# Kernel optimization log

Hardware: AMD Instinct MI355X
Metric: run time of the kernel (lower is better)

Reference implementation:

```python
import jax, jax.numpy as jnp
import numpy as np

B, V, F, H = 2, 5023, 9976, 256
CHUNK = 128
EPS = 1e-5
LIGHT_LOC = jnp.array([0.0, 1.0, 3.0], dtype=jnp.float32)   # PointLights(location)
AMB, DIFF, SPEC = 0.5, 0.3, 0.2 * 0.6                        # light amb/diff * mat(1.0); spec light*mat
SHININESS = 10.0
TEXEL = jnp.array([142.0, 179.0, 247.0], dtype=jnp.float32) / 255.0
BG = jnp.array([1.0, 1.0, 1.0], dtype=jnp.float32)


def setup_inputs():
    key = jax.random.key(0)
    k1, k2 = jax.random.split(key)
    vertices = jax.random.normal(k1, (B, V, 3), dtype=jnp.float32) * 0.05
    faces = jax.random.randint(k2, (F, 3), 0, V)
    # default camera built inside forward: R = diag(-1,1,-1), T = (0,0,2*scale)
    tm = jnp.array([[-1.0, 0.0, 0.0, 0.0],
                    [0.0, 1.0, 0.0, 0.0],
                    [0.0, 0.0, -1.0, 2.0]], dtype=jnp.float32)
    transform_matrix = jnp.tile(tm[None], (B, 1, 1))
    focal_length = jnp.full((B, 1), 12.0, dtype=jnp.float32)
    return {"vertices": vertices, "transform_matrix": transform_matrix,
            "focal_length": focal_length, "faces": faces}


def _normalize(v):
    return v / jnp.maximum(jnp.linalg.norm(v, axis=-1, keepdims=True), 1e-6)


def _render(vertices, transform_matrix, focal_length, faces):
    R = transform_matrix[:, :3, :3]
    T = transform_matrix[:, :3, 3]
    # pytorch3d row-vector convention: x_cam = x_world @ R + T
    verts_cam = jnp.einsum('bvi,bij->bvj', vertices, R) + T[:, None, :]
    zc = verts_cam[..., 2]                                    # view depth
    x_ndc = focal_length * verts_cam[..., 0] / zc             # fx*x/z (+px=0)
    y_ndc = focal_length * verts_cam[..., 1] / zc
    vndc = jnp.stack([x_ndc, y_ndc, zc], axis=-1)             # [B,V,3]

    # pixel centers in pytorch3d NDC (+x left, +y up); top-left pixel -> (+1-1/H, +1-1/H)
    ax = 1.0 - (2.0 * jnp.arange(H, dtype=jnp.float32) + 1.0) / H
    px = jnp.tile(ax[None, :], (H, 1)).reshape(-1)            # [P] columns
    py = jnp.tile(ax[:, None], (1, H)).reshape(-1)            # [P] rows
    P = H * H

    npad = (-F) % CHUNK
    faces_p = jnp.concatenate([faces, jnp.zeros((npad, 3), faces.dtype)], 0)
    fvalid = jnp.concatenate([jnp.ones((F,), bool), jnp.zeros((npad,), bool)])
    n_chunks = faces_p.shape[0] // CHUNK
    chunk_ids = jnp.arange(n_chunks * CHUNK, dtype=jnp.int32).reshape(n_chunks, CHUNK)

    def step(carry, fidx):
        best_z, bw0, bw1, bw2, best_face = carry
        tri = faces_p[fidx]                                   # [C,3]
        fv = vndc[:, tri]                                     # [B,C,3,3]
        def corner(k):
            return (fv[:, :, k, 0][..., None], fv[:, :, k, 1][..., None],
                    fv[:, :, k, 2][..., None])
        x0, y0, z0 = corner(0); x1, y1, z1 = corner(1); x2, y2, z2 = corner(2)
        z0s = jnp.where(z0 > EPS, z0, 1.0)
        z1s = jnp.where(z1 > EPS, z1, 1.0)
        z2s = jnp.where(z2 > EPS, z2, 1.0)
        den = (y1 - y2) * (x0 - x2) + (x2 - x1) * (y0 - y2)   # [B,C,1]
        ok = jnp.abs(den) > 1e-8
        dens = jnp.where(ok, den, 1.0)
        w0 = ((y1 - y2) * (px - x2) + (x2 - x1) * (py - y2)) / dens   # [B,C,P]
        w1 = ((y2 - y0) * (px - x2) + (x0 - x2) * (py - y2)) / dens
        w2 = 1.0 - w0 - w1
        inside = (w0 >= 0) & (w1 >= 0) & (w2 >= 0) & ok
        inside &= (z0 > EPS) & (z1 > EPS) & (z2 > EPS)
        inside &= fvalid[fidx][None, :, None]
        iz = w0 / z0s + w1 / z1s + w2 / z2s                    # perspective-correct 1/z
        good = inside & (iz > 1e-8)
        izs = jnp.where(good, iz, 1.0)
        zsafe = 1.0 / izs
        zpix = jnp.where(good, zsafe, jnp.inf)
        w0c = jnp.where(good, (w0 / z0s) * zsafe, 0.0)
        w1c = jnp.where(good, (w1 / z1s) * zsafe, 0.0)
        w2c = jnp.where(good, (w2 / z2s) * zsafe, 0.0)
        idx = jnp.argmin(zpix, axis=1)                         # [B,P]
        g = lambda a: jnp.take_along_axis(a, idx[:, None, :], axis=1)[:, 0]
        zmin = g(zpix)
        upd = zmin < best_z
        best_z = jnp.where(upd, zmin, best_z)
        bw0 = jnp.where(upd, g(w0c), bw0)
        bw1 = jnp.where(upd, g(w1c), bw1)
        bw2 = jnp.where(upd, g(w2c), bw2)
        best_face = jnp.where(upd, fidx[idx], best_face)
        return (best_z, bw0, bw1, bw2, best_face), None

    init = (jnp.full((B, P), jnp.inf, jnp.float32),
            jnp.zeros((B, P), jnp.float32), jnp.zeros((B, P), jnp.float32),
            jnp.zeros((B, P), jnp.float32), jnp.full((B, P), -1, jnp.int32))
    (best_z, bw0, bw1, bw2, best_face), _ = jax.lax.scan(jax.checkpoint(step), init, chunk_ids)

    mask = best_face >= 0                                      # [B,P]
    bary = jnp.stack([bw0, bw1, bw2], axis=-1)                 # [B,P,3]
    tri_sel = faces_p[jnp.clip(best_face, 0)]                  # [B,P,3]

    # area-weighted vertex normals (pytorch3d _compute_vertex_normals)
    fw = vertices[:, faces]                                    # [B,F,3,3]
    fn = jnp.cross(fw[:, :, 1] - fw[:, :, 0], fw[:, :, 2] - fw[:, :, 0])  # [B,F,3]
    vn = jnp.zeros_like(vertices).at[:, faces.reshape(-1)].add(jnp.repeat(fn, 3, axis=1))
    vn = _normalize(vn)

    gv = jax.vmap(lambda t, i: t[i])(vertices, tri_sel)        # [B,P,3,3] world pos
    gn = jax.vmap(lambda t, i: t[i])(vn, tri_sel)              # [B,P,3,3] normals
    pos = jnp.einsum('bpk,bpkc->bpc', bary, gv)
    nrm = _normalize(jnp.einsum('bpk,bpkc->bpc', bary, gn))

    cam_pos = -jnp.einsum('bj,bkj->bk', T, R)                  # camera center in world
    Ldir = _normalize(LIGHT_LOC - pos)
    Vdir = _normalize(cam_pos[:, None, :] - pos)
    cosNL = jnp.sum(nrm * Ldir, axis=-1)
    diffuse = DIFF * jax.nn.relu(cosNL)
    refl = 2.0 * cosNL[..., None] * nrm - Ldir
    spec = SPEC * jax.nn.relu(jnp.sum(Vdir * refl, axis=-1)) ** SHININESS
    rgb = TEXEL * (AMB + diffuse)[..., None] + spec[..., None] # [B,P,3]
    rgb = jnp.where(mask[..., None], rgb, BG)                  # hard_rgb_blend, bg=(1,1,1)

    images = rgb.reshape(B, H, H, 3).transpose(0, 3, 1, 2) * 255.0  # area-interp to same size = identity
    alpha = mask.astype(jnp.float32).reshape(B, 1, H, H)
    return images, alpha


def reference(vertices, transform_matrix, focal_length, faces):
    return _render(vertices, transform_matrix, focal_length, faces)
```

## Files before the change

### kernel.cpp

```cpp
#include <hip/hip_runtime.h>
#include <stdint.h>

#define H 256
#define PIX (H*H)
#define BATCH 2
#define NV 5023
#define NF 9976
#define EPS 1e-5f
#define CH 128
#define NBUCK 4096

typedef unsigned long long ull;
#define INF_KEY 0x7F800000FFFFFFFFULL

__device__ __forceinline__ float axf(int i) {
    return 1.0f - (2.0f * (float)i + 1.0f) / (float)H;
}

__device__ __forceinline__ float bf16snap(float x) {
    unsigned u = __float_as_uint(x);
    unsigned r = (u + 0x7FFFu + ((u >> 16) & 1u)) & 0xFFFF0000u;
    return __uint_as_float(r);
}

__device__ __forceinline__ int zbucket(float z) {
    int q = (int)floorf((z - 0.5f) * (4096.0f / 3.0f));
    return q < 0 ? 0 : (q > 4095 ? 4095 : q);
}
__device__ __forceinline__ float zbucket_lower(int q) {
    return (q == 0) ? 0.0f : 0.5f + (float)q * (3.0f / 4096.0f);
}

__global__ void face_setup(const float* __restrict__ verts, const float* __restrict__ tm,
                           const float* __restrict__ focal, const int* __restrict__ faces,
                           float* __restrict__ fd, float* __restrict__ zminArr) {
#pragma clang fp contract(off)
    int t = blockIdx.x * blockDim.x + threadIdx.x;
    if (t >= BATCH * NF) return;
    int b = t / NF, f = t % NF;
    const float* M = tm + b * 12;
    float fl = focal[b];
    float X[3], Y[3], Z[3];
#pragma unroll
    for (int k = 0; k < 3; k++) {
        int vi = faces[f * 3 + k];
        const float* v = verts + (b * NV + vi) * 3;
        float v0 = v[0], v1 = v[1], v2 = v[2];
        float c0 = ((v0 * M[0] + v1 * M[4]) + v2 * M[8])  + M[3];
        float c1 = ((v0 * M[1] + v1 * M[5]) + v2 * M[9])  + M[7];
        float c2 = ((v0 * M[2] + v1 * M[6]) + v2 * M[10]) + M[11];
        X[k] = (fl * c0) / c2;
        Y[k] = (fl * c1) / c2;
        Z[k] = c2;
    }
    float x0 = X[0], x1 = X[1], x2 = X[2];
    float y0 = Y[0], y1 = Y[1], y2 = Y[2];
    float z0 = Z[0], z1 = Z[1], z2 = Z[2];
    float den = (y1 - y2) * (x0 - x2) + (x2 - x1) * (y0 - y2);
    bool zv = (z0 > EPS) && (z1 > EPS) && (z2 > EPS);
    bool okS = zv && (fabsf(den) > 1e-8f);
    bool okR = zv && (fabsf(den) > 5e-9f);
    float xmn, xmx, ymn, ymx;
    if (okR) {
        float e01 = (x1 - x0) * (x1 - x0) + (y1 - y0) * (y1 - y0);
        float e12 = (x2 - x1) * (x2 - x1) + (y2 - y1) * (y2 - y1);
        float e20 = (x0 - x2) * (x0 - x2) + (y0 - y2) * (y0 - y2);
        float E2 = fmaxf(fmaxf(e01, e12), e20);
        float delta = 1e-4f * E2 / fabsf(den) + 1e-3f;
        if (!(delta < 4.0f)) delta = 4.0f;
        xmn = fminf(fminf(x0, x1), x2) - delta;
        xmx = fmaxf(fmaxf(x0, x1), x2) + delta;
        ymn = fminf(fminf(y0, y1), y2) - delta;
        ymx = fmaxf(fmaxf(y0, y1), y2) + delta;
    } else {
        xmn = 1e30f; xmx = -1e30f; ymn = 1e30f; ymx = -1e30f;
    }
    float* o = fd + (size_t)t * 16;
    o[0] = y1 - y2;  o[1] = x2 - x1;
    o[2] = y2 - y0;  o[3] = x0 - x2;
    o[4] = x2;       o[5] = y2;
    o[6] = den;      o[7] = okS ? 1.0f : 0.0f;
    o[8] = xmn;  o[9] = xmx;  o[10] = ymn;  o[11] = ymx;
    o[12] = z0;  o[13] = z1;  o[14] = z2;   o[15] = 0.0f;
    zminArr[t] = okR ? fminf(fminf(z0, z1), z2) : -1.0f;
}

__global__ void fn_scatter(const float* __restrict__ verts, const int* __restrict__ faces,
                           float* __restrict__ vn) {
#pragma clang fp contract(off)
    int t = blockIdx.x * blockDim.x + threadIdx.x;
    if (t >= BATCH * NF) return;
    int b = t / NF, f = t % NF;
    int i0 = faces[f*3+0], i1 = faces[f*3+1], i2 = faces[f*3+2];
    const float* vb = verts + b * NV * 3;
    float a0 = vb[i0*3+0], a1 = vb[i0*3+1], a2 = vb[i0*3+2];
    float b0 = vb[i1*3+0], b1 = vb[i1*3+1], b2 = vb[i1*3+2];
    float c0 = vb[i2*3+0], c1 = vb[i2*3+1], c2 = vb[i2*3+2];
    float e1x = b0 - a0, e1y = b1 - a1, e1z = b2 - a2;
    float e2x = c0 - a0, e2y = c1 - a1, e2z = c2 - a2;
    float nx = e1y * e2z - e1z * e2y;
    float ny = e1z * e2x - e1x * e2z;
    float nz = e1x * e2y - e1y * e2x;
    float* nb = vn + (size_t)b * NV * 3;
    atomicAdd(&nb[i0*3+0], nx); atomicAdd(&nb[i0*3+1], ny); atomicAdd(&nb[i0*3+2], nz);
    atomicAdd(&nb[i1*3+0], nx); atomicAdd(&nb[i1*3+1], ny); atomicAdd(&nb[i1*3+2], nz);
    atomicAdd(&nb[i2*3+0], nx); atomicAdd(&nb[i2*3+1], ny); atomicAdd(&nb[i2*3+2], nz);
}

__global__ void vn_normalize(float* __restrict__ vn) {
#pragma clang fp contract(off)
    int t = blockIdx.x * blockDim.x + threadIdx.x;
    if (t >= BATCH * NV) return;
    float x = vn[t*3+0], y = vn[t*3+1], z = vn[t*3+2];
    float n = fmaxf(sqrtf((x*x + y*y) + z*z), 1e-6f);
    vn[t*3+0] = x / n; vn[t*3+1] = y / n; vn[t*3+2] = z / n;
}

__global__ void zhist(const float* __restrict__ zminArr, int* __restrict__ hist) {
    int t = blockIdx.x * blockDim.x + threadIdx.x;
    if (t >= BATCH * NF) return;
    float zm = zminArr[t];
    if (zm < 0.0f) return;
    int b = t / NF;
    atomicAdd(&hist[b * NBUCK + zbucket(zm)], 1);
}

__global__ __launch_bounds__(256) void zscan(const int* __restrict__ hist,
                                             int* __restrict__ start,
                                             int* __restrict__ total) {
    int b = blockIdx.x;
    __shared__ int tot[256];
    int t = threadIdx.x;
    int a[16]; int s = 0;
#pragma unroll
    for (int i = 0; i < 16; i++) { int c = hist[b * NBUCK + t * 16 + i]; a[i] = s; s += c; }
    tot[t] = s;
    __syncthreads();
    for (int off = 1; off < 256; off <<= 1) {
        int x = tot[t];
        if (t >= off) x += tot[t - off];
        __syncthreads();
        tot[t] = x;
        __syncthreads();
    }
    int pre = (t > 0) ? tot[t - 1] : 0;
#pragma unroll
    for (int i = 0; i < 16; i++) start[b * NBUCK + t * 16 + i] = pre + a[i];
    if (t == 255) total[b] = tot[255];
}

__global__ void zscatter(const float* __restrict__ fd, const float* __restrict__ zminArr,
                         const int* __restrict__ start, int* __restrict__ cursor,
                         float* __restrict__ fds, float* __restrict__ blow) {
    int t = blockIdx.x * blockDim.x + threadIdx.x;
    if (t >= BATCH * NF) return;
    float zm = zminArr[t];
    if (zm < 0.0f) return;
    int b = t / NF, f = t % NF;
    int q = zbucket(zm);
    int dst = start[b * NBUCK + q] + atomicAdd(&cursor[b * NBUCK + q], 1);
    const float* o = fd + (size_t)t * 16;
    float* d = fds + ((size_t)b * NF + dst) * 16;
#pragma unroll
    for (int k = 0; k < 15; k++) d[k] = o[k];
    d[15] = __uint_as_float((unsigned)f);
    blow[(size_t)b * NF + dst] = zbucket_lower(q);
}

__global__ __launch_bounds__(64) void raster(const float* __restrict__ fds,
                                             const float* __restrict__ blow,
                                             const int* __restrict__ total,
                                             int2* __restrict__ pix) {
#pragma clang fp contract(off)
    __shared__ __align__(16) float sfd[CH * 16];
    __shared__ int slist[CH];
    __shared__ int scnt;
    int tid = threadIdx.x;
    int b = blockIdx.z;
    int col0 = blockIdx.x * 8, row0 = blockIdx.y * 8;
    int col = col0 + (tid & 7), row = row0 + (tid >> 3);
    float px = axf(col), py = axf(row);
    float qxmax = axf(col0), qxmin = axf(col0 + 7);
    float qymax = axf(row0), qymin = axf(row0 + 7);
    ull ks = INF_KEY, k1 = INF_KEY, k2 = INF_KEY;
    const float4* fdb4 = (const float4*)(fds + (size_t)b * NF * 16);
    int cntb = total[b];

    for (int fbase = 0; fbase < cntb; fbase += CH) {
        int n = min(CH, cntb - fbase);
        if (tid == 0) scnt = 0;
        for (int j = tid; j < n * 4; j += 64)
            ((float4*)sfd)[j] = fdb4[(size_t)fbase * 4 + j];
        __syncthreads();
        for (int j = tid; j < n; j += 64) {
            const float* o = sfd + j * 16;
            if (o[8] <= qxmax && o[9] >= qxmin && o[10] <= qymax && o[11] >= qymin) {
                int p2 = atomicAdd(&scnt, 1);
                slist[p2] = j;
            }
        }
        __syncthreads();
        int cnt = scnt;
        for (int i = 0; i < cnt; i++) {
            const float* o = sfd + slist[i] * 16;
            bool cand = (px >= o[8]) & (px <= o[9]) & (py >= o[10]) & (py <= o[11]);
            if (__ballot(cand) == 0ULL) continue;
            float dx = px - o[4], dy = py - o[5];
            float w0 = (o[0] * dx + o[1] * dy) / o[6];
            float w1 = (o[2] * dx + o[3] * dy) / o[6];
            float w2 = (1.0f - w0) - w1;
            bool insS = cand && (o[7] != 0.0f) && (w0 >= 0.0f) && (w1 >= 0.0f) && (w2 >= 0.0f);
            bool insR = cand && (w0 >= -1e-5f) && (w1 >= -1e-5f) && (w2 >= -1e-5f);
            if (__ballot(insR) == 0ULL) continue;
            float iz = ((w0 / o[12]) + (w1 / o[13])) + (w2 / o[14]);
            if (insR && (iz > 1e-8f)) {
                float zp = 1.0f / iz;
                ull key = ((ull)__float_as_uint(zp) << 32) |
                          (ull)(unsigned)__float_as_uint(o[15]);
                if (insS && key < ks) ks = key;
                if (key < k1) { k2 = k1; k1 = key; }
                else if (key < k2) { k2 = key; }
            }
        }
        if (fbase + CH < cntb) {
            float nf = blow[(size_t)b * NF + fbase + CH];
            float madj = nf * (1.0f - 1e-4f);
            float zsv = __uint_as_float((unsigned)(ks >> 32));
            float zbv = __uint_as_float((unsigned)(k2 >> 32));
            bool oldc = (ks != INF_KEY) && (k2 != INF_KEY) && (zsv < madj) && (zbv < madj);
            bool newc = (ks != INF_KEY) && (1.051f * zsv < madj);
            bool done = (nf > 0.0f) && (oldc || newc);
            if (__ballot(!done) == 0ULL) break;
            __syncthreads();
        }
    }
    int fs = -1;
    float zs = 0.0f;
    if ((unsigned)(ks >> 32) != 0x7F800000u) {
        fs = (int)(unsigned)ks;
        zs = __uint_as_float((unsigned)(ks >> 32));
    }
    int fr = -1;
    if (fs >= 0) {
        ull mR = INF_KEY;
        if ((int)(unsigned)k1 != fs && k1 < mR) mR = k1;
        if ((int)(unsigned)k2 != fs && k2 < mR) mR = k2;
        if ((unsigned)(mR >> 32) != 0x7F800000u) {
            float zr = __uint_as_float((unsigned)(mR >> 32));
            if (fabsf(zr - zs) <= 0.05f * zs) fr = (int)(unsigned)mR;
        }
    }
    pix[(size_t)b * PIX + (size_t)row * H + col] = make_int2(fs, fr);
}

__device__ void shade_face(int f, int b, float px, float py,
                           const float* __restrict__ fd, const float* __restrict__ verts,
                           const int* __restrict__ faces, const float* __restrict__ vn,
                           const float* __restrict__ tm, float* rgb) {
#pragma clang fp contract(off)
    const float* o = fd + ((size_t)b * NF + f) * 16;
    float dx = px - o[4], dy = py - o[5];
    float w0 = (o[0] * dx + o[1] * dy) / o[6];
    float w1 = (o[2] * dx + o[3] * dy) / o[6];
    float w2 = (1.0f - w0) - w1;
    float q0 = w0 / o[12], q1 = w1 / o[13], q2 = w2 / o[14];
    float iz = (q0 + q1) + q2;
    float zsafe = 1.0f / iz;
    float bw0 = q0 * zsafe, bw1 = q1 * zsafe, bw2 = q2 * zsafe;
    int i0 = faces[f*3+0], i1 = faces[f*3+1], i2 = faces[f*3+2];
    const float* vb = verts + b * NV * 3;
    const float* nb = vn + b * NV * 3;
    float posx = (bw0*vb[i0*3+0] + bw1*vb[i1*3+0]) + bw2*vb[i2*3+0];
    float posy = (bw0*vb[i0*3+1] + bw1*vb[i1*3+1]) + bw2*vb[i2*3+1];
    float posz = (bw0*vb[i0*3+2] + bw1*vb[i1*3+2]) + bw2*vb[i2*3+2];
    float nx = (bw0*nb[i0*3+0] + bw1*nb[i1*3+0]) + bw2*nb[i2*3+0];
    float ny = (bw0*nb[i0*3+1] + bw1*nb[i1*3+1]) + bw2*nb[i2*3+1];
    float nz = (bw0*nb[i0*3+2] + bw1*nb[i1*3+2]) + bw2*nb[i2*3+2];
    float nn = fmaxf(sqrtf((nx*nx + ny*ny) + nz*nz), 1e-6f);
    nx /= nn; ny /= nn; nz /= nn;
    const float* M = tm + b * 12;
    float T0 = M[3], T1 = M[7], T2 = M[11];
    float cpx = -((T0*M[0] + T1*M[1]) + T2*M[2]);
    float cpy = -((T0*M[4] + T1*M[5]) + T2*M[6]);
    float cpz = -((T0*M[8] + T1*M[9]) + T2*M[10]);
    float lx = 0.0f - posx, ly = 1.0f - posy, lz = 3.0f - posz;
    float ln = fmaxf(sqrtf((lx*lx + ly*ly) + lz*lz), 1e-6f);
    lx /= ln; ly /= ln; lz /= ln;
    float vx = cpx - posx, vy = cpy - posy, vz = cpz - posz;
    float vnn = fmaxf(sqrtf((vx*vx + vy*vy) + vz*vz), 1e-6f);
    vx /= vnn; vy /= vnn; vz /= vnn;
    float cosNL = (nx*lx + ny*ly) + nz*lz;
    float diffuse = 0.3f * fmaxf(cosNL, 0.0f);
    float rx = (2.0f * cosNL) * nx - lx;
    float ry = (2.0f * cosNL) * ny - ly;
    float rz = (2.0f * cosNL) * nz - lz;
    float vr = (vx*rx + vy*ry) + vz*rz;
    float spec = 0.12f * powf(fmaxf(vr, 0.0f), 10.0f);
    float sA = 0.5f + diffuse;
    rgb[0] = ((142.0f / 255.0f) * sA + spec) * 255.0f;
    rgb[1] = ((179.0f / 255.0f) * sA + spec) * 255.0f;
    rgb[2] = ((247.0f / 255.0f) * sA + spec) * 255.0f;
}

__global__ void shade(const int2* __restrict__ pix, const float* __restrict__ fd,
                      const float* __restrict__ verts, const int* __restrict__ faces,
                      const float* __restrict__ vn, const float* __restrict__ tm,
                      float* __restrict__ out) {
#pragma clang fp contract(off)
    int t = blockIdx.x * blockDim.x + threadIdx.x;
    if (t >= BATCH * PIX) return;
    int b = t / PIX, p = t % PIX;
    int row = p / H, col = p % H;
    int2 pk = pix[t];
    int fs = pk.x, fr = pk.y;
    float r, g, bc, a;
    if (fs < 0) {
        r = g = bc = 255.0f;
        a = 0.0f;
    } else {
        float px = axf(col), py = axf(row);
        float A[3];
        shade_face(fs, b, px, py, fd, verts, faces, vn, tm, A);
        r = A[0]; g = A[1]; bc = A[2];
        if (fr >= 0) {
            float Bc[3];
            shade_face(fr, b, px, py, fd, verts, faces, vn, tm, Bc);
            float As0 = bf16snap(A[0]), As1 = bf16snap(A[1]), As2 = bf16snap(A[2]);
            float Bs0 = bf16snap(Bc[0]), Bs1 = bf16snap(Bc[1]), Bs2 = bf16snap(Bc[2]);
            if (fabsf(As0 - Bs0) <= 9.01f && fabsf(As1 - Bs1) <= 9.01f &&
                fabsf(As2 - Bs2) <= 9.01f) {
                r  = 0.5f * (As0 + Bs0);
                g  = 0.5f * (As1 + Bs1);
                bc = 0.5f * (As2 + Bs2);
            }
        }
        a = 1.0f;
    }
    out[(((size_t)b*3 + 0) * H + row) * H + col] = r;
    out[(((size_t)b*3 + 1) * H + row) * H + col] = g;
    out[(((size_t)b*3 + 2) * H + row) * H + col] = bc;
    out[(size_t)BATCH*3*H*H + ((size_t)b * H + row) * H + col] = a;
}

extern "C" void kernel_launch(void* const* d_in, const int* in_sizes, int n_in,
                              void* d_out, int out_size, void* d_ws, size_t ws_size,
                              hipStream_t stream) {
    const float* verts = (const float*)d_in[0];
    const float* tm    = (const float*)d_in[1];
    const float* focal = (const float*)d_in[2];
    const int*   faces = (const int*)d_in[3];
    float* out = (float*)d_out;

    char* ws = (char*)d_ws;
    float* fd      = (float*)ws;
    float* vn      = (float*)(ws + 1276928);
    int2*  pix     = (int2*) (ws + 1397504);
    float* fds     = (float*)(ws + 2446080);
    float* blow    = (float*)(ws + 3723008);
    float* zminArr = (float*)(ws + 3802880);
    int*   hist    = (int*)  (ws + 3882752);
    int*   start   = (int*)  (ws + 3915520);
    int*   cursor  = (int*)  (ws + 3948288);
    int*   total   = (int*)  (ws + 3981056);

    hipMemsetAsync(vn, 0, (size_t)BATCH * NV * 3 * sizeof(float), stream);
    hipMemsetAsync(hist, 0, (size_t)BATCH * NBUCK * sizeof(int), stream);
    hipMemsetAsync(cursor, 0, (size_t)BATCH * NBUCK * sizeof(int), stream);

    face_setup<<<(BATCH * NF + 255) / 256, 256, 0, stream>>>(verts, tm, focal, faces, fd, zminArr);
    fn_scatter<<<(BATCH * NF + 255) / 256, 256, 0, stream>>>(verts, faces, vn);
    vn_normalize<<<(BATCH * NV + 255) / 256, 256, 0, stream>>>(vn);

    zhist<<<(BATCH * NF + 255) / 256, 256, 0, stream>>>(zminArr, hist);
    zscan<<<BATCH, 256, 0, stream>>>(hist, start, total);
    zscatter<<<(BATCH * NF + 255) / 256, 256, 0, stream>>>(fd, zminArr, start, cursor, fds, blow);

    dim3 rg(32, 32, BATCH);
    raster<<<rg, 64, 0, stream>>>(fds, blow, total, pix);

    shade<<<(BATCH * PIX + 255) / 256, 256, 0, stream>>>(pix, fd, verts, faces, vn, tm, out);
}
```

Measured before the change: 343.4 us.

## Fuse setup kernels, merge memsets, and load only culled face data in raster

Face setup, normal scatter and the z-histogram are merged into one kernel, and vertex-normal normalization moves into zscatter. The workspace is rearranged so vn, hist and cursor sit next to each other and are cleared by a single memset, which removes several launches and memsets. In raster, only the bounding boxes are loaded first, and full face records are gathered into compacted shared memory only for faces that pass the tile cull, cutting shared-memory fill traffic. This adds an extra barrier per chunk and relies on kernel ordering so that normalization runs after all normal atomics have finished.

```diff
diff --git a/kernel.cpp b/kernel.cpp
--- a/kernel.cpp
+++ b/kernel.cpp
@@ -31,9 +31,10 @@
     return (q == 0) ? 0.0f : 0.5f + (float)q * (3.0f / 4096.0f);
 }
 
-__global__ void face_setup(const float* __restrict__ verts, const float* __restrict__ tm,
-                           const float* __restrict__ focal, const int* __restrict__ faces,
-                           float* __restrict__ fd, float* __restrict__ zminArr) {
+__global__ void setup_all(const float* __restrict__ verts, const float* __restrict__ tm,
+                          const float* __restrict__ focal, const int* __restrict__ faces,
+                          float* __restrict__ fd, float* __restrict__ zminArr,
+                          float* __restrict__ vn, int* __restrict__ hist) {
 #pragma clang fp contract(off)
     int t = blockIdx.x * blockDim.x + threadIdx.x;
     if (t >= BATCH * NF) return;
@@ -82,47 +83,26 @@
     o[6] = den;      o[7] = okS ? 1.0f : 0.0f;
     o[8] = xmn;  o[9] = xmx;  o[10] = ymn;  o[11] = ymx;
     o[12] = z0;  o[13] = z1;  o[14] = z2;   o[15] = 0.0f;
-    zminArr[t] = okR ? fminf(fminf(z0, z1), z2) : -1.0f;
-}
-
-__global__ void fn_scatter(const float* __restrict__ verts, const int* __restrict__ faces,
-                           float* __restrict__ vn) {
-#pragma clang fp contract(off)
-    int t = blockIdx.x * blockDim.x + threadIdx.x;
-    if (t >= BATCH * NF) return;
-    int b = t / NF, f = t % NF;
-    int i0 = faces[f*3+0], i1 = faces[f*3+1], i2 = faces[f*3+2];
-    const float* vb = verts + b * NV * 3;
-    float a0 = vb[i0*3+0], a1 = vb[i0*3+1], a2 = vb[i0*3+2];
-    float b0 = vb[i1*3+0], b1 = vb[i1*3+1], b2 = vb[i1*3+2];
-    float c0 = vb[i2*3+0], c1 = vb[i2*3+1], c2 = vb[i2*3+2];
-    float e1x = b0 - a0, e1y = b1 - a1, e1z = b2 - a2;
-    float e2x = c0 - a0, e2y = c1 - a1, e2z = c2 - a2;
-    float nx = e1y * e2z - e1z * e2y;
-    float ny = e1z * e2x - e1x * e2z;
-    float nz = e1x * e2y - e1y * e2x;
-    float* nb = vn + (size_t)b * NV * 3;
-    atomicAdd(&nb[i0*3+0], nx); atomicAdd(&nb[i0*3+1], ny); atomicAdd(&nb[i0*3+2], nz);
-    atomicAdd(&nb[i1*3+0], nx); atomicAdd(&nb[i1*3+1], ny); atomicAdd(&nb[i1*3+2], nz);
-    atomicAdd(&nb[i2*3+0], nx); atomicAdd(&nb[i2*3+1], ny); atomicAdd(&nb[i2*3+2], nz);
-}
-
-__global__ void vn_normalize(float* __restrict__ vn) {
-#pragma clang fp contract(off)
-    int t = blockIdx.x * blockDim.x + threadIdx.x;
-    if (t >= BATCH * NV) return;
-    float x = vn[t*3+0], y = vn[t*3+1], z = vn[t*3+2];
-    float n = fmaxf(sqrtf((x*x + y*y) + z*z), 1e-6f);
-    vn[t*3+0] = x / n; vn[t*3+1] = y / n; vn[t*3+2] = z / n;
-}
-
-__global__ void zhist(const float* __restrict__ zminArr, int* __restrict__ hist) {
-    int t = blockIdx.x * blockDim.x + threadIdx.x;
-    if (t >= BATCH * NF) return;
-    float zm = zminArr[t];
-    if (zm < 0.0f) return;
-    int b = t / NF;
-    atomicAdd(&hist[b * NBUCK + zbucket(zm)], 1);
+    float zm = okR ? fminf(fminf(z0, z1), z2) : -1.0f;
+    zminArr[t] = zm;
+    if (zm >= 0.0f) atomicAdd(&hist[b * NBUCK + zbucket(zm)], 1);
+
+    {
+        int i0 = faces[f*3+0], i1 = faces[f*3+1], i2 = faces[f*3+2];
+        const float* vb = verts + b * NV * 3;
+        float a0 = vb[i0*3+0], a1 = vb[i0*3+1], a2 = vb[i0*3+2];
+        float b0 = vb[i1*3+0], b1 = vb[i1*3+1], b2 = vb[i1*3+2];
+        float c0 = vb[i2*3+0], c1 = vb[i2*3+1], c2 = vb[i2*3+2];
+        float e1x = b0 - a0, e1y = b1 - a1, e1z = b2 - a2;
+        float e2x = c0 - a0, e2y = c1 - a1, e2z = c2 - a2;
+        float nx = e1y * e2z - e1z * e2y;
+        float ny = e1z * e2x - e1x * e2z;
+        float nz = e1x * e2y - e1y * e2x;
+        float* nb = vn + (size_t)b * NV * 3;
+        atomicAdd(&nb[i0*3+0], nx); atomicAdd(&nb[i0*3+1], ny); atomicAdd(&nb[i0*3+2], nz);
+        atomicAdd(&nb[i1*3+0], nx); atomicAdd(&nb[i1*3+1], ny); atomicAdd(&nb[i1*3+2], nz);
+        atomicAdd(&nb[i2*3+0], nx); atomicAdd(&nb[i2*3+1], ny); atomicAdd(&nb[i2*3+2], nz);
+    }
 }
 
 __global__ __launch_bounds__(256) void zscan(const int* __restrict__ hist,
@@ -151,8 +131,15 @@
 
 __global__ void zscatter(const float* __restrict__ fd, const float* __restrict__ zminArr,
                          const int* __restrict__ start, int* __restrict__ cursor,
-                         float* __restrict__ fds, float* __restrict__ blow) {
+                         float* __restrict__ fds, float* __restrict__ blow,
+                         float* __restrict__ vn) {
+#pragma clang fp contract(off)
     int t = blockIdx.x * blockDim.x + threadIdx.x;
+    if (t < BATCH * NV) {
+        float x = vn[t*3+0], y = vn[t*3+1], z = vn[t*3+2];
+        float n = fmaxf(sqrtf((x*x + y*y) + z*z), 1e-6f);
+        vn[t*3+0] = x / n; vn[t*3+1] = y / n; vn[t*3+2] = z / n;
+    }
     if (t >= BATCH * NF) return;
     float zm = zminArr[t];
     if (zm < 0.0f) return;
@@ -172,6 +159,7 @@
                                              const int* __restrict__ total,
                                              int2* __restrict__ pix) {
 #pragma clang fp contract(off)
+    __shared__ __align__(16) float4 sbb[CH];
     __shared__ __align__(16) float sfd[CH * 16];
     __shared__ int slist[CH];
     __shared__ int scnt;
@@ -189,20 +177,25 @@
     for (int fbase = 0; fbase < cntb; fbase += CH) {
         int n = min(CH, cntb - fbase);
         if (tid == 0) scnt = 0;
-        for (int j = tid; j < n * 4; j += 64)
-            ((float4*)sfd)[j] = fdb4[(size_t)fbase * 4 + j];
+        for (int j = tid; j < n; j += 64)
+            sbb[j] = fdb4[(size_t)(fbase + j) * 4 + 2];
         __syncthreads();
         for (int j = tid; j < n; j += 64) {
-            const float* o = sfd + j * 16;
-            if (o[8] <= qxmax && o[9] >= qxmin && o[10] <= qymax && o[11] >= qymin) {
+            float4 bb = sbb[j];
+            if (bb.x <= qxmax && bb.y >= qxmin && bb.z <= qymax && bb.w >= qymin) {
                 int p2 = atomicAdd(&scnt, 1);
                 slist[p2] = j;
             }
         }
         __syncthreads();
         int cnt = scnt;
+        for (int j = tid; j < cnt * 4; j += 64) {
+            int e = fbase + slist[j >> 2];
+            ((float4*)sfd)[j] = fdb4[(size_t)e * 4 + (j & 3)];
+        }
+        __syncthreads();
         for (int i = 0; i < cnt; i++) {
-            const float* o = sfd + slist[i] * 16;
+            const float* o = sfd + i * 16;
             bool cand = (px >= o[8]) & (px <= o[9]) & (py >= o[10]) & (py <= o[11]);
             if (__ballot(cand) == 0ULL) continue;
             float dx = px - o[4], dy = py - o[5];
@@ -354,27 +347,22 @@
     char* ws = (char*)d_ws;
     float* fd      = (float*)ws;
     float* vn      = (float*)(ws + 1276928);
-    int2*  pix     = (int2*) (ws + 1397504);
-    float* fds     = (float*)(ws + 2446080);
-    float* blow    = (float*)(ws + 3723008);
-    float* zminArr = (float*)(ws + 3802880);
-    int*   hist    = (int*)  (ws + 3882752);
-    int*   start   = (int*)  (ws + 3915520);
-    int*   cursor  = (int*)  (ws + 3948288);
+    int*   hist    = (int*)  (ws + 1397504);
+    int*   cursor  = (int*)  (ws + 1430272);
+    int2*  pix     = (int2*) (ws + 1463040);
+    float* fds     = (float*)(ws + 2511616);
+    float* blow    = (float*)(ws + 3788544);
+    float* zminArr = (float*)(ws + 3868416);
+    int*   start   = (int*)  (ws + 3948288);
     int*   total   = (int*)  (ws + 3981056);
 
-    hipMemsetAsync(vn, 0, (size_t)BATCH * NV * 3 * sizeof(float), stream);
-    hipMemsetAsync(hist, 0, (size_t)BATCH * NBUCK * sizeof(int), stream);
-    hipMemsetAsync(cursor, 0, (size_t)BATCH * NBUCK * sizeof(int), stream);
-
-    face_setup<<<(BATCH * NF + 255) / 256, 256, 0, stream>>>(verts, tm, focal, faces, fd, zminArr);
-    fn_scatter<<<(BATCH * NF + 255) / 256, 256, 0, stream>>>(verts, faces, vn);
-    vn_normalize<<<(BATCH * NV + 255) / 256, 256, 0, stream>>>(vn);
-
-    zhist<<<(BATCH * NF + 255) / 256, 256, 0, stream>>>(zminArr, hist);
+    hipMemsetAsync(vn, 0, 186112, stream);
+
+    setup_all<<<(BATCH * NF + 255) / 256, 256, 0, stream>>>(verts, tm, focal, faces,
+                                                            fd, zminArr, vn, hist);
     zscan<<<BATCH, 256, 0, stream>>>(hist, start, total);
-    zscatter<<<(BATCH * NF + 255) / 256, 256, 0, stream>>>(fd, zminArr, start, cursor, fds, blow);
-
+    zscatter<<<(BATCH * NF + 255) / 256, 256, 0, stream>>>(fd, zminArr, start, cursor,
+                                                           fds, blow, vn);
     dim3 rg(32, 32, BATCH);
     raster<<<rg, 64, 0, stream>>>(fds, blow, total, pix);
 
```

After: 318.3 us. -7.3%, faster.
